# Kernel optimization log

Measured on AMD Instinct MI355X. Metric: run time of the kernel, lower is better.

The kernel has to match this reference:

```python
import jax, jax.numpy as jnp
import numpy as np

N, P, H, W = 4, 16, 384, 384   # batch, stroke samples, canvas rows/cols
K = 8                          # spline knots -> K-1 segments
BH = BW = 64                   # brush sprite size


def setup_inputs() -> dict:
    key = jax.random.key(0)
    ks = jax.random.split(key, 9)
    images = jax.random.uniform(ks[0], (N, 4, H, W), jnp.float32)
    knot_t = jnp.arange(K, dtype=jnp.float32)
    # segment start values a: x,y inside canvas, z (pressure) in (0.2, 1.0]
    xy = jax.random.uniform(ks[1], (N, K - 1, 2), jnp.float32) * 220.0 + 80.0
    z = jax.random.uniform(ks[2], (N, K - 1, 1), jnp.float32) * 0.8 + 0.2
    a = jnp.concatenate([xy, z], axis=-1)
    b = jax.random.normal(ks[3], (N, K - 1, 3), jnp.float32) * jnp.array([30.0, 30.0, 0.1], jnp.float32)
    two_c = jax.random.normal(ks[4], (N, K - 1, 3), jnp.float32) * jnp.array([5.0, 5.0, 0.02], jnp.float32)
    three_d = jax.random.normal(ks[5], (N, K - 1, 3), jnp.float32) * jnp.array([2.0, 2.0, 0.01], jnp.float32)
    colors = jax.random.uniform(ks[6], (N, 4), jnp.float32)
    ts = jnp.sort(jax.random.uniform(ks[7], (P,), jnp.float32) * (K - 1))
    brush = jax.random.uniform(ks[8], (4, BH, BW), jnp.float32)
    return {"images": images, "knot_t": knot_t, "a": a, "b": b, "two_c": two_c,
            "three_d": three_d, "colors": colors, "ts": ts, "brush": brush}


def _spline_eval(knot_t, a, b, two_c, three_d, ts):
    # torchcubicspline NaturalCubicSpline: x(f) = a + b f + (two_c/2) f^2 + (three_d/3) f^3
    idx = jnp.clip(jnp.searchsorted(knot_t, ts, side="right") - 1, 0, knot_t.shape[0] - 2)  # (P,)
    f = (ts - knot_t[idx])[None, :, None]                       # (1,P,1)
    a_, b_, c_, d_ = a[:, idx], b[:, idx], two_c[:, idx], three_d[:, idx]  # (N,P,3)
    q = a_ + (b_ + (c_ / 2.0 + d_ * f / 3.0) * f) * f
    qd = b_ + (c_ + d_ * f) * f
    return q, qd


def _draw_sprite(brush_p, x, y, theta, s):
    # brush_p: (4, BH+2, BW+2) zero-padded sprite; blit at pose (x,y,theta) with scale s -> (4,H,W)
    rows = jnp.arange(H, dtype=jnp.float32)[:, None]
    cols = jnp.arange(W, dtype=jnp.float32)[None, :]
    dx, dy = cols - x, rows - y
    ct, st = jnp.cos(theta), jnp.sin(theta)
    u = (ct * dx + st * dy) / s + (BW - 1) / 2.0 + 1.0   # +1: pad offset
    v = (-st * dx + ct * dy) / s + (BH - 1) / 2.0 + 1.0
    u0, v0 = jnp.floor(u), jnp.floor(v)
    du, dv = u - u0, v - v0
    u0i = jnp.clip(u0.astype(jnp.int32), 0, BW + 1)
    u1i = jnp.clip(u0i + 1, 0, BW + 1)
    v0i = jnp.clip(v0.astype(jnp.int32), 0, BH + 1)
    v1i = jnp.clip(v0i + 1, 0, BH + 1)
    g = lambda vi, ui: brush_p[:, vi, ui]                 # gather -> (4,H,W)
    return (g(v0i, u0i) * (1 - du) * (1 - dv) + g(v0i, u1i) * du * (1 - dv)
            + g(v1i, u0i) * (1 - du) * dv + g(v1i, u1i) * du * dv)


def reference(images, knot_t, a, b, two_c, three_d, colors, ts, brush):
    q, qd = _spline_eval(knot_t, a, b, two_c, three_d, ts)    # (N,P,3)
    x, y = q[..., 0], q[..., 1]
    theta = -jnp.arctan2(qd[..., 1], qd[..., 0])
    s = jnp.clip(q[..., 2], 0.001, 1.0)
    # per-batch colored brush: rgb channels <- color, alpha scaled by color alpha
    rgb = jnp.broadcast_to(colors[:, :3, None, None], (N, 3, BH, BW))
    alpha = jnp.broadcast_to(brush[None, 3:], (N, 1, BH, BW)) * colors[:, 3, None, None, None]
    brush_b = jnp.concatenate([rgb, alpha], axis=1)           # (N,4,BH,BW)
    brush_p = jnp.pad(brush_b, ((0, 0), (0, 0), (1, 1), (1, 1)))  # zero border = transparent outside
    draw = jax.vmap(jax.vmap(_draw_sprite, in_axes=(None, 0, 0, 0, 0)),
                    in_axes=(0, 0, 0, 0, 0))
    sprites = draw(brush_p, x, y, theta, s)                   # (N,P,4,H,W)
    # oil-paint colorspace: subtractive, p = 1 - v (b2p == p2b == 1-x)
    sprites_oil = 1.0 - sprites
    alphas = 1.0 - sprites_oil[:, :, 3:]                      # sprite alpha     (N,P,1,H,W)
    inv = sprites_oil[:, :, 3:]                               # 1 - alpha
    scaled = sprites_oil[:, :, :3] * alphas                   # premultiplied paint
    active = (q[..., 2] > 0)[:, :, None, None, None]          # z > 0 gate per point
    inv = jnp.where(active, inv, 1.0)
    scaled = jnp.where(active, scaled, 0.0)
    # sequential alpha-over vectorized via suffix products:
    # final = img0 * prod_j inv_j + sum_k scaled_k * prod_{j>k} inv_j
    T_incl = jnp.cumprod(inv[:, ::-1], axis=1)[:, ::-1]       # prod_{j>=k}
    T_excl = jnp.concatenate([T_incl[:, 1:], jnp.ones_like(T_incl[:, :1])], axis=1)
    img0 = 1.0 - images[:, :3]                                # b2p of canvas rgb
    final = img0 * T_incl[:, 0] + jnp.sum(scaled * T_excl, axis=1)
    return 1.0 - final                                        # p2b -> (N,3,H,W)
```

## Files before the change

kernel.cpp:

```cpp
#include <hip/hip_runtime.h>
#include <math.h>

#pragma clang fp contract(off)

namespace {
constexpr int P_STR  = 16;
constexpr int K_KNOT = 8;
constexpr int H = 384;
constexpr int W = 384;
constexpr int BH = 64;
constexpr int BW = 64;
constexpr int TW = 32;
constexpr int TH = 8;
constexpr int PAD = 66;
constexpr int LDSP = 67;
constexpr int AFLOATS = 66 * LDSP + 2;
constexpr int PARAM_F = 8;
constexpr int ALPHA_BASE = 512;
}

__device__ __forceinline__ float fdlibm_atanf_plain(float x)
{
#pragma clang fp contract(off)
    const float atanhi0 = 4.6364760399e-01f, atanhi1 = 7.8539812565e-01f,
                atanhi2 = 9.8279368877e-01f, atanhi3 = 1.5707962513e+00f;
    const float atanlo0 = 5.0121582440e-09f, atanlo1 = 3.7748947079e-08f,
                atanlo2 = 3.4473217170e-08f, atanlo3 = 7.5497894159e-08f;
    const float aT0 = 3.3333328366e-01f, aT1 = -1.9999158382e-01f,
                aT2 = 1.4253635705e-01f, aT3 = -1.0648017377e-01f,
                aT4 = 6.1687607318e-02f;
    const float one = 1.0f;

    const int hx = __float_as_int(x);
    const int ix = hx & 0x7fffffff;
    int id;
    if (ix >= 0x4c800000) {
        if (ix > 0x7f800000) return x + x;
        return (hx > 0) ? (atanhi3 + atanlo3) : (-atanhi3 - atanlo3);
    }
    if (ix < 0x3ee00000) {
        if (ix < 0x39800000) return x;
        id = -1;
    } else {
        x = fabsf(x);
        if (ix < 0x3f980000) {
            if (ix < 0x3f300000) {
                id = 0; x = (2.0f * x - one) / (2.0f + x);
            } else {
                id = 1; x = (x - one) / (x + one);
            }
        } else {
            if (ix < 0x401c0000) {
                id = 2; x = (x - 1.5f) / (one + 1.5f * x);
            } else {
                id = 3; x = -1.0f / x;
            }
        }
    }
    const float z = x * x;
    const float w = z * z;
    const float s1 = z * (aT0 + w * (aT2 + w * aT4));
    const float s2 = w * (aT1 + w * aT3);
    if (id < 0) return x - x * (s1 + s2);
    const float ahi = (id == 0) ? atanhi0 : (id == 1) ? atanhi1 : (id == 2) ? atanhi2 : atanhi3;
    const float alo = (id == 0) ? atanlo0 : (id == 1) ? atanlo1 : (id == 2) ? atanlo2 : atanlo3;
    const float zz = ahi - ((x * (s1 + s2) - alo) - x);
    return (hx < 0) ? -zz : zz;
}

__device__ __forceinline__ float fdlibm_atan2f_plain(float y, float x)
{
#pragma clang fp contract(off)
    const float pi_o_2 = 1.5707963705e+00f;
    const float pi_    = 3.1415927410e+00f;
    const float pi_lo  = -8.7422776573e-08f;

    const int hx = __float_as_int(x), hy = __float_as_int(y);
    const int ix = hx & 0x7fffffff, iy = hy & 0x7fffffff;
    if (ix > 0x7f800000 || iy > 0x7f800000) return x + y;
    if (hx == 0x3f800000) return fdlibm_atanf_plain(y);
    int m = ((hy >> 31) & 1) | ((hx >> 30) & 2);

    if (iy == 0) {
        switch (m) {
            case 0: case 1: return y;
            case 2: return pi_;
            default: return -pi_;
        }
    }
    if (ix == 0) return (hy < 0) ? -pi_o_2 : pi_o_2;
    if (ix == 0x7f800000) {
        if (iy == 0x7f800000) {
            switch (m) {
                case 0: return  pi_o_2 * 0.5f;
                case 1: return -pi_o_2 * 0.5f;
                case 2: return  3.0f * pi_o_2 * 0.5f;
                default: return -3.0f * pi_o_2 * 0.5f;
            }
        }
        switch (m) {
            case 0: return 0.0f;
            case 1: return -0.0f;
            case 2: return pi_;
            default: return -pi_;
        }
    }
    if (iy == 0x7f800000) return (hy < 0) ? -pi_o_2 : pi_o_2;

    const int k = (iy - ix) >> 23;
    float z;
    if (k > 26) {
        z = pi_o_2 + 0.5f * pi_lo;
        m &= 1;
    } else if (hx < 0 && k < -26) {
        z = 0.0f;
    } else {
        z = fdlibm_atanf_plain(fabsf(y / x));
    }
    switch (m) {
        case 0: return z;
        case 1: return -z;
        case 2: return pi_ - (z - pi_lo);
        default: return (z - pi_lo) - pi_;
    }
}

__global__ __launch_bounds__(256) void param_kernel(
    const float* __restrict__ knot_t, const float* __restrict__ a_,
    const float* __restrict__ b_,     const float* __restrict__ c2_,
    const float* __restrict__ d3_,    const float* __restrict__ colors,
    const float* __restrict__ ts,     const float* __restrict__ brush,
    float* __restrict__ ws)
{
#pragma clang fp contract(off)
    const int n   = blockIdx.x;
    const int tid = threadIdx.x;

    if (tid < P_STR) {
        const int p = tid;
        const float t = ts[p];
        int ins = 0;
        #pragma unroll
        for (int i = 0; i < K_KNOT; ++i) ins += (knot_t[i] <= t) ? 1 : 0;
        const int idx = min(max(ins - 1, 0), K_KNOT - 2);
        const float f = t - knot_t[idx];

        const int base = (n * (K_KNOT - 1) + idx) * 3;
        const float C3INV = 0.3333333432674408f;
        float q[3], qd[3];
        #pragma unroll
        for (int j = 0; j < 3; ++j) {
            const float aj = a_[base + j], bj = b_[base + j];
            const float cj = c2_[base + j], dj = d3_[base + j];
            const float inner = cj * 0.5f + (dj * f) * C3INV;
            q[j]  = aj + (bj + inner * f) * f;
            qd[j] = bj + (cj + dj * f) * f;
        }
        const float x = q[0], y = q[1], z = q[2];
        const float s = fminf(fmaxf(z, 0.001f), 1.0f);

        const float apos = fdlibm_atan2f_plain(qd[1], qd[0]);
        const float thf  = -apos;
        const float ct_  = (float)cos((double)thf);
        const float st_  = (float)sin((double)thf);

        float* P = ws + (size_t)(n * P_STR + p) * PARAM_F;
        P[0] = x; P[1] = y; P[2] = 1.0f / s;
        P[3] = ct_; P[4] = st_;
        P[5] = (z > 0.0f) ? 1.0f : 0.0f;
        P[6] = 0.0f; P[7] = 0.0f;
    }

    const float c3 = colors[n * 4 + 3];
    float* A = ws + ALPHA_BASE + (size_t)n * AFLOATS;
    for (int i = tid; i < AFLOATS; i += 256) {
        const int v = i / LDSP;
        const int u = i - v * LDSP;
        float val = 0.0f;
        if ((unsigned)(v - 1) < (unsigned)BH && (unsigned)(u - 1) < (unsigned)BW)
            val = brush[3 * BH * BW + (v - 1) * BW + (u - 1)] * c3;
        A[i] = val;
    }
}

__global__ __launch_bounds__(256) void blit_kernel(
    const float* __restrict__ images, const float* __restrict__ colors,
    const float* __restrict__ ws,     float* __restrict__ out)
{
#pragma clang fp contract(off)
    __shared__ float sP[P_STR * PARAM_F];
    __shared__ __align__(8) float s_alpha[AFLOATS];
    __shared__ int   sCull[P_STR];

    const int n   = blockIdx.z;
    const int c0  = blockIdx.x * TW;
    const int r0  = blockIdx.y * TH;
    const int tid = threadIdx.x;

    if (tid < P_STR * PARAM_F)
        sP[tid] = ws[(size_t)n * P_STR * PARAM_F + tid];
    __syncthreads();

    if (tid < P_STR) {
        const float* P = sP + tid * PARAM_F;
        int keep = 0;
        if (P[5] > 0.0f) {
            const double x = (double)P[0], y = (double)P[1], rs = (double)P[2];
            const double ct = (double)P[3], st = (double)P[4];
            const double cLo = (double)c0, cHi = (double)(c0 + TW - 1);
            const double rLo = (double)r0, rHi = (double)(r0 + TH - 1);
            const double cu = (ct >= 0.0) ? cLo : cHi;
            const double ru = (st >= 0.0) ? rLo : rHi;
            const double umin = (ct * (cu - x) + st * (ru - y)) * rs + 32.5;
            const double cv = (st <= 0.0) ? cLo : cHi;
            const double rv = (ct >= 0.0) ? rLo : rHi;
            const double vmin = (-st * (cv - x) + ct * (rv - y)) * rs + 32.5;
            keep = (umin < 66.0 && vmin < 66.0) ? 1 : 0;
        }
        sCull[tid] = keep;
    }

    {
        const float2* src = reinterpret_cast<const float2*>(ws + ALPHA_BASE + (size_t)n * AFLOATS);
        float2* dst = reinterpret_cast<float2*>(s_alpha);
        #pragma unroll
        for (int i = 0; i < AFLOATS / 2; i += 256) {
            const int k = i + tid;
            if (k < AFLOATS / 2) dst[k] = src[k];
        }
    }
    __syncthreads();

    unsigned mask = 0;
    #pragma unroll
    for (int p = 0; p < P_STR; ++p) mask |= (sCull[p] ? (1u << p) : 0u);

    const int row = tid >> 5;
    const int col = tid & 31;
    const int r   = r0 + row;
    const int c   = c0 + col;
    const float rf  = (float)r;
    const float cjf = (float)c;

    const float col0 = colors[n * 4 + 0];
    const float col1 = colors[n * 4 + 1];
    const float col2 = colors[n * 4 + 2];

    const size_t pix = (size_t)r * W + c;
    const size_t imgbase = ((size_t)n * 4) * H * W + pix;
    float F0 = 1.0f - images[imgbase];
    float F1 = 1.0f - images[imgbase + (size_t)H * W];
    float F2 = 1.0f - images[imgbase + 2 * (size_t)H * W];

    for (int p = 0; p < P_STR; ++p) {
        if (!((mask >> p) & 1u)) continue;
        const float* P = sP + p * PARAM_F;
        const float x  = P[0], y = P[1], rs = P[2];
        const float ct = P[3], st = P[4];
        const float nst = -st;
        const float dy  = rf - y;
        const float tu  = st * dy;
        const float tv  = ct * dy;
        const float dx  = cjf - x;

        float u = (ct * dx + tu) * rs;
        u = u + 31.5f; u = u + 1.0f;
        float v = (nst * dx + tv) * rs;
        v = v + 31.5f; v = v + 1.0f;

        const float u0f = floorf(u), v0f = floorf(v);
        const float du = u - u0f, dv = v - v0f;
        const int ui = (int)u0f, vi = (int)v0f;
        const int u0c = min(max(ui, 0), PAD - 1);
        const int u1c = min(u0c + 1, PAD - 1);
        const int v0c = min(max(vi, 0), PAD - 1);
        const int v1c = min(v0c + 1, PAD - 1);

        const float inu0 = ((unsigned)(u0c - 1) < 64u) ? 1.0f : 0.0f;
        const float inu1 = ((unsigned)(u1c - 1) < 64u) ? 1.0f : 0.0f;
        const float inv0 = ((unsigned)(v0c - 1) < 64u) ? 1.0f : 0.0f;
        const float inv1 = ((unsigned)(v1c - 1) < 64u) ? 1.0f : 0.0f;
        const float mu = inu0 + du * (inu1 - inu0);
        const float mv = inv0 + dv * (inv1 - inv0);
        const float M  = mu * mv;

        const int b0 = v0c * LDSP, b1 = v1c * LDSP;
        const float a00 = s_alpha[b0 + u0c], a01 = s_alpha[b0 + u1c];
        const float a10 = s_alpha[b1 + u0c], a11 = s_alpha[b1 + u1c];
        const float ax0 = a00 + du * (a01 - a00);
        const float ax1 = a10 + du * (a11 - a10);
        const float av  = ax0 + dv * (ax1 - ax0);

        const float inva = 1.0f - av;
        const float am   = av * M;
        F0 = F0 * inva + (av - col0 * am);
        F1 = F1 * inva + (av - col1 * am);
        F2 = F2 * inva + (av - col2 * am);
    }

    const size_t outbase = ((size_t)n * 3) * H * W + pix;
    out[outbase]                     = 1.0f - F0;
    out[outbase + (size_t)H * W]     = 1.0f - F1;
    out[outbase + 2 * (size_t)H * W] = 1.0f - F2;
}

extern "C" void kernel_launch(void* const* d_in, const int* in_sizes, int n_in,
                              void* d_out, int out_size, void* d_ws, size_t ws_size,
                              hipStream_t stream) {
    (void)in_sizes; (void)n_in; (void)ws_size; (void)out_size;
    const float* images = (const float*)d_in[0];
    const float* knot_t = (const float*)d_in[1];
    const float* a_     = (const float*)d_in[2];
    const float* b_     = (const float*)d_in[3];
    const float* c2_    = (const float*)d_in[4];
    const float* d3_    = (const float*)d_in[5];
    const float* colors = (const float*)d_in[6];
    const float* ts     = (const float*)d_in[7];
    const float* brush  = (const float*)d_in[8];
    float* out = (float*)d_out;
    float* ws  = (float*)d_ws;

    hipLaunchKernelGGL(param_kernel, dim3(4), dim3(256), 0, stream,
                       knot_t, a_, b_, c2_, d3_, colors, ts, brush, ws);
    hipLaunchKernelGGL(blit_kernel, dim3(W / TW, H / TH, 4), dim3(256), 0, stream,
                       images, colors, ws, out);
}
```

Measured before the change: 24.52 us.

## Precompute per-tile cull masks in param kernel and skip LDS staging for empty tiles

Moves the per-tile stroke culling test from each blit block into the param kernel, which writes one bitmask per tile to the workspace. Blit blocks read their mask and skip loading the brush alpha table and the param array into LDS when no stroke touches the tile. Tiles become 32x16 and each thread handles two adjacent pixels with float2 loads and stores. The param kernel runs with only 4 blocks and now does double-precision culling for all tiles, which could lengthen that serial stage.

```diff
diff --git a/kernel.cpp b/kernel.cpp
--- a/kernel.cpp
+++ b/kernel.cpp
@@ -11,12 +11,16 @@
 constexpr int BH = 64;
 constexpr int BW = 64;
 constexpr int TW = 32;
-constexpr int TH = 8;
+constexpr int TH = 16;
+constexpr int NTX = W / TW;
+constexpr int NTY = H / TH;
+constexpr int NTILES = NTX * NTY;
 constexpr int PAD = 66;
 constexpr int LDSP = 67;
 constexpr int AFLOATS = 66 * LDSP + 2;
 constexpr int PARAM_F = 8;
-constexpr int ALPHA_BASE = 512;
+constexpr int MASK_BASE = 512;
+constexpr int ALPHA_BASE = 2048;
 }
 
 __device__ __forceinline__ float fdlibm_atanf_plain(float x)
@@ -133,6 +137,9 @@
     float* __restrict__ ws)
 {
 #pragma clang fp contract(off)
+    __shared__ float hX[P_STR], hY[P_STR], hRs[P_STR], hCt[P_STR], hSt[P_STR];
+    __shared__ int   hAct[P_STR];
+
     const int n   = blockIdx.x;
     const int tid = threadIdx.x;
 
@@ -163,12 +170,40 @@
         const float thf  = -apos;
         const float ct_  = (float)cos((double)thf);
         const float st_  = (float)sin((double)thf);
+        const float rs_  = 1.0f / s;
 
         float* P = ws + (size_t)(n * P_STR + p) * PARAM_F;
-        P[0] = x; P[1] = y; P[2] = 1.0f / s;
+        P[0] = x; P[1] = y; P[2] = rs_;
         P[3] = ct_; P[4] = st_;
         P[5] = (z > 0.0f) ? 1.0f : 0.0f;
         P[6] = 0.0f; P[7] = 0.0f;
+
+        hX[p] = x; hY[p] = y; hRs[p] = rs_; hCt[p] = ct_; hSt[p] = st_;
+        hAct[p] = (z > 0.0f) ? 1 : 0;
+    }
+    __syncthreads();
+
+    unsigned* wmask = reinterpret_cast<unsigned*>(ws) + MASK_BASE + n * NTILES;
+    for (int t = tid; t < NTILES; t += 256) {
+        const int tx = t % NTX, ty = t / NTX;
+        const double cLo = (double)(tx * TW), cHi = (double)(tx * TW + TW - 1);
+        const double rLo = (double)(ty * TH), rHi = (double)(ty * TH + TH - 1);
+        unsigned m = 0;
+        #pragma unroll
+        for (int p = 0; p < P_STR; ++p) {
+            if (!hAct[p]) continue;
+            const double x = (double)hX[p], y = (double)hY[p];
+            const double rs = (double)hRs[p];
+            const double ct = (double)hCt[p], st = (double)hSt[p];
+            const double cu = (ct >= 0.0) ? cLo : cHi;
+            const double ru = (st >= 0.0) ? rLo : rHi;
+            const double umin = (ct * (cu - x) + st * (ru - y)) * rs + 32.5;
+            const double cv = (st <= 0.0) ? cLo : cHi;
+            const double rv = (ct >= 0.0) ? rLo : rHi;
+            const double vmin = (-st * (cv - x) + ct * (rv - y)) * rs + 32.5;
+            if (umin < 66.0 && vmin < 66.0) m |= (1u << p);
+        }
+        wmask[t] = m;
     }
 
     const float c3 = colors[n * 4 + 3];
@@ -190,118 +225,111 @@
 #pragma clang fp contract(off)
     __shared__ float sP[P_STR * PARAM_F];
     __shared__ __align__(8) float s_alpha[AFLOATS];
-    __shared__ int   sCull[P_STR];
 
     const int n   = blockIdx.z;
-    const int c0  = blockIdx.x * TW;
-    const int r0  = blockIdx.y * TH;
+    const int bx  = blockIdx.x, by = blockIdx.y;
+    const int c0  = bx * TW;
+    const int r0  = by * TH;
     const int tid = threadIdx.x;
 
-    if (tid < P_STR * PARAM_F)
-        sP[tid] = ws[(size_t)n * P_STR * PARAM_F + tid];
-    __syncthreads();
-
-    if (tid < P_STR) {
-        const float* P = sP + tid * PARAM_F;
-        int keep = 0;
-        if (P[5] > 0.0f) {
-            const double x = (double)P[0], y = (double)P[1], rs = (double)P[2];
-            const double ct = (double)P[3], st = (double)P[4];
-            const double cLo = (double)c0, cHi = (double)(c0 + TW - 1);
-            const double rLo = (double)r0, rHi = (double)(r0 + TH - 1);
-            const double cu = (ct >= 0.0) ? cLo : cHi;
-            const double ru = (st >= 0.0) ? rLo : rHi;
-            const double umin = (ct * (cu - x) + st * (ru - y)) * rs + 32.5;
-            const double cv = (st <= 0.0) ? cLo : cHi;
-            const double rv = (ct >= 0.0) ? rLo : rHi;
-            const double vmin = (-st * (cv - x) + ct * (rv - y)) * rs + 32.5;
-            keep = (umin < 66.0 && vmin < 66.0) ? 1 : 0;
-        }
-        sCull[tid] = keep;
-    }
-
-    {
-        const float2* src = reinterpret_cast<const float2*>(ws + ALPHA_BASE + (size_t)n * AFLOATS);
-        float2* dst = reinterpret_cast<float2*>(s_alpha);
-        #pragma unroll
-        for (int i = 0; i < AFLOATS / 2; i += 256) {
-            const int k = i + tid;
-            if (k < AFLOATS / 2) dst[k] = src[k];
-        }
-    }
-    __syncthreads();
-
-    unsigned mask = 0;
-    #pragma unroll
-    for (int p = 0; p < P_STR; ++p) mask |= (sCull[p] ? (1u << p) : 0u);
-
-    const int row = tid >> 5;
-    const int col = tid & 31;
+    const unsigned mask =
+        reinterpret_cast<const unsigned*>(ws)[MASK_BASE + n * NTILES + by * NTX + bx];
+
+    const int row = tid >> 4;
+    const int cp  = tid & 15;
     const int r   = r0 + row;
-    const int c   = c0 + col;
-    const float rf  = (float)r;
-    const float cjf = (float)c;
-
-    const float col0 = colors[n * 4 + 0];
-    const float col1 = colors[n * 4 + 1];
-    const float col2 = colors[n * 4 + 2];
+    const int c   = c0 + cp * 2;
+    const float rf = (float)r;
 
     const size_t pix = (size_t)r * W + c;
-    const size_t imgbase = ((size_t)n * 4) * H * W + pix;
-    float F0 = 1.0f - images[imgbase];
-    float F1 = 1.0f - images[imgbase + (size_t)H * W];
-    float F2 = 1.0f - images[imgbase + 2 * (size_t)H * W];
-
-    for (int p = 0; p < P_STR; ++p) {
-        if (!((mask >> p) & 1u)) continue;
-        const float* P = sP + p * PARAM_F;
-        const float x  = P[0], y = P[1], rs = P[2];
-        const float ct = P[3], st = P[4];
-        const float nst = -st;
-        const float dy  = rf - y;
-        const float tu  = st * dy;
-        const float tv  = ct * dy;
-        const float dx  = cjf - x;
-
-        float u = (ct * dx + tu) * rs;
-        u = u + 31.5f; u = u + 1.0f;
-        float v = (nst * dx + tv) * rs;
-        v = v + 31.5f; v = v + 1.0f;
-
-        const float u0f = floorf(u), v0f = floorf(v);
-        const float du = u - u0f, dv = v - v0f;
-        const int ui = (int)u0f, vi = (int)v0f;
-        const int u0c = min(max(ui, 0), PAD - 1);
-        const int u1c = min(u0c + 1, PAD - 1);
-        const int v0c = min(max(vi, 0), PAD - 1);
-        const int v1c = min(v0c + 1, PAD - 1);
-
-        const float inu0 = ((unsigned)(u0c - 1) < 64u) ? 1.0f : 0.0f;
-        const float inu1 = ((unsigned)(u1c - 1) < 64u) ? 1.0f : 0.0f;
-        const float inv0 = ((unsigned)(v0c - 1) < 64u) ? 1.0f : 0.0f;
-        const float inv1 = ((unsigned)(v1c - 1) < 64u) ? 1.0f : 0.0f;
-        const float mu = inu0 + du * (inu1 - inu0);
-        const float mv = inv0 + dv * (inv1 - inv0);
-        const float M  = mu * mv;
-
-        const int b0 = v0c * LDSP, b1 = v1c * LDSP;
-        const float a00 = s_alpha[b0 + u0c], a01 = s_alpha[b0 + u1c];
-        const float a10 = s_alpha[b1 + u0c], a11 = s_alpha[b1 + u1c];
-        const float ax0 = a00 + du * (a01 - a00);
-        const float ax1 = a10 + du * (a11 - a10);
-        const float av  = ax0 + dv * (ax1 - ax0);
-
-        const float inva = 1.0f - av;
-        const float am   = av * M;
-        F0 = F0 * inva + (av - col0 * am);
-        F1 = F1 * inva + (av - col1 * am);
-        F2 = F2 * inva + (av - col2 * am);
-    }
-
-    const size_t outbase = ((size_t)n * 3) * H * W + pix;
-    out[outbase]                     = 1.0f - F0;
-    out[outbase + (size_t)H * W]     = 1.0f - F1;
-    out[outbase + 2 * (size_t)H * W] = 1.0f - F2;
+    const size_t hw  = (size_t)H * W;
+    const size_t imgbase = ((size_t)n * 4) * hw + pix;
+
+    const float2 i0 = *reinterpret_cast<const float2*>(images + imgbase);
+    const float2 i1 = *reinterpret_cast<const float2*>(images + imgbase + hw);
+    const float2 i2 = *reinterpret_cast<const float2*>(images + imgbase + 2 * hw);
+    float F0[2] = {1.0f - i0.x, 1.0f - i0.y};
+    float F1[2] = {1.0f - i1.x, 1.0f - i1.y};
+    float F2[2] = {1.0f - i2.x, 1.0f - i2.y};
+
+    if (mask) {
+        if (tid < P_STR * PARAM_F)
+            sP[tid] = ws[(size_t)n * P_STR * PARAM_F + tid];
+        {
+            const float2* src = reinterpret_cast<const float2*>(
+                ws + ALPHA_BASE + (size_t)n * AFLOATS);
+            float2* dst = reinterpret_cast<float2*>(s_alpha);
+            #pragma unroll
+            for (int i = 0; i < AFLOATS / 2; i += 256) {
+                const int k = i + tid;
+                if (k < AFLOATS / 2) dst[k] = src[k];
+            }
+        }
+        __syncthreads();
+
+        const float col0 = colors[n * 4 + 0];
+        const float col1 = colors[n * 4 + 1];
+        const float col2 = colors[n * 4 + 2];
+
+        for (int p = 0; p < P_STR; ++p) {
+            if (!((mask >> p) & 1u)) continue;
+            const float* P = sP + p * PARAM_F;
+            const float x  = P[0], y = P[1], rs = P[2];
+            const float ct = P[3], st = P[4];
+            const float nst = -st;
+            const float dy  = rf - y;
+            const float tu  = st * dy;
+            const float tv  = ct * dy;
+
+            #pragma unroll
+            for (int j = 0; j < 2; ++j) {
+                const float cjf = (float)(c + j);
+                const float dx  = cjf - x;
+                float u = (ct * dx + tu) * rs;
+                u = u + 31.5f; u = u + 1.0f;
+                float v = (nst * dx + tv) * rs;
+                v = v + 31.5f; v = v + 1.0f;
+
+                const float u0f = floorf(u), v0f = floorf(v);
+                const float du = u - u0f, dv = v - v0f;
+                const int ui = (int)u0f, vi = (int)v0f;
+                const int u0c = min(max(ui, 0), PAD - 1);
+                const int u1c = min(u0c + 1, PAD - 1);
+                const int v0c = min(max(vi, 0), PAD - 1);
+                const int v1c = min(v0c + 1, PAD - 1);
+
+                const float inu0 = ((unsigned)(u0c - 1) < 64u) ? 1.0f : 0.0f;
+                const float inu1 = ((unsigned)(u1c - 1) < 64u) ? 1.0f : 0.0f;
+                const float inv0 = ((unsigned)(v0c - 1) < 64u) ? 1.0f : 0.0f;
+                const float inv1 = ((unsigned)(v1c - 1) < 64u) ? 1.0f : 0.0f;
+                const float mu = inu0 + du * (inu1 - inu0);
+                const float mv = inv0 + dv * (inv1 - inv0);
+                const float M  = mu * mv;
+
+                const int b0 = v0c * LDSP, b1 = v1c * LDSP;
+                const float a00 = s_alpha[b0 + u0c], a01 = s_alpha[b0 + u1c];
+                const float a10 = s_alpha[b1 + u0c], a11 = s_alpha[b1 + u1c];
+                const float ax0 = a00 + du * (a01 - a00);
+                const float ax1 = a10 + du * (a11 - a10);
+                const float av  = ax0 + dv * (ax1 - ax0);
+
+                const float inva = 1.0f - av;
+                const float am   = av * M;
+                F0[j] = F0[j] * inva + (av - col0 * am);
+                F1[j] = F1[j] * inva + (av - col1 * am);
+                F2[j] = F2[j] * inva + (av - col2 * am);
+            }
+        }
+    }
+
+    const size_t outbase = ((size_t)n * 3) * hw + pix;
+    float2 o0, o1, o2;
+    o0.x = 1.0f - F0[0]; o0.y = 1.0f - F0[1];
+    o1.x = 1.0f - F1[0]; o1.y = 1.0f - F1[1];
+    o2.x = 1.0f - F2[0]; o2.y = 1.0f - F2[1];
+    *reinterpret_cast<float2*>(out + outbase)          = o0;
+    *reinterpret_cast<float2*>(out + outbase + hw)     = o1;
+    *reinterpret_cast<float2*>(out + outbase + 2 * hw) = o2;
 }
 
 extern "C" void kernel_launch(void* const* d_in, const int* in_sizes, int n_in,
@@ -322,6 +350,6 @@
 
     hipLaunchKernelGGL(param_kernel, dim3(4), dim3(256), 0, stream,
                        knot_t, a_, b_, c2_, d3_, colors, ts, brush, ws);
-    hipLaunchKernelGGL(blit_kernel, dim3(W / TW, H / TH, 4), dim3(256), 0, stream,
+    hipLaunchKernelGGL(blit_kernel, dim3(NTX, NTY, 4), dim3(256), 0, stream,
                        images, colors, ws, out);
 }
```

Result: slower. 28.24 us (+15.2%).
